# Performance work log

Hardware: AMD Instinct MI355X
Metric: run time of the kernel (lower is better)

## Reference

```python
import jax, jax.numpy as jnp
import numpy as np

THRESH = 0.2  # contact probability threshold from _make_graph default


def setup_inputs() -> dict:
    key = jax.random.key(0)
    ks = jax.random.split(key, 10)
    L, D, K, M = 1024, 640, 32, 64
    S = jax.random.normal(ks[0], (L, D), jnp.float32)
    P = jax.random.uniform(ks[1], (L, L), jnp.float32)
    P = 0.5 * (P + P.T)  # symmetric base-pair probability matrix
    xyz = jax.random.normal(ks[2], (L, 3), jnp.float32) * 10.0  # Angstrom-scale C1' coords
    rbf_mu = jnp.linspace(0.0, 30.0, K).astype(jnp.float32)     # RBF centers over 0-30 A
    rbf_sigma = jax.random.uniform(ks[3], (K,), jnp.float32, 0.5, 2.0)
    W_edge = jax.random.normal(ks[4], (K + 2, M), jnp.float32) * 0.05
    b_edge = jnp.zeros((M,), jnp.float32)
    W_node = jax.random.normal(ks[5], (D, M), jnp.float32) * 0.05
    w_out = jax.random.normal(ks[6], (M,), jnp.float32) * 0.1
    return {"S": S, "P": P, "xyz": xyz, "rbf_mu": rbf_mu, "rbf_sigma": rbf_sigma,
            "W_edge": W_edge, "b_edge": b_edge, "W_node": W_node, "w_out": w_out}


def reference(S, P, xyz, rbf_mu, rbf_sigma, W_edge, b_edge, W_node, w_out):
    """Graph construction (_make_graph) + one SE3-style gated coordinate update.

    Edges: backbone (j == i+1, etype=0, pij=1) and high-prob contacts
    (P[i,j] > THRESH, j > i+2, etype=1, pij=P[i,j]). Edge scalars are
    [etype, pij, rbf(d)] exactly as in _make_graph; edge vectors are
    xyz[j]-xyz[i]. Computed in dense masked form for jit-compatibility.
    """
    L = xyz.shape[0]
    rel = xyz[None, :, :] - xyz[:, None, :]                      # (L,L,3) xyz[j]-xyz[i]
    # safe norm: eps avoids nan grad on zero diagonal (diagonal is masked out anyway)
    d = jnp.sqrt(jnp.sum(rel * rel, axis=-1, keepdims=True) + 1e-12)  # (L,L,1)
    rbf_feat = jnp.exp(-(d - rbf_mu) ** 2 / (2.0 * rbf_sigma ** 2))   # (L,L,K)

    idx = jnp.arange(L)
    backbone = idx[None, :] == idx[:, None] + 1                  # j == i+1
    contact = (P > THRESH) & (idx[None, :] > idx[:, None] + 2)   # skip j <= i+2
    mask = backbone | contact                                    # (L,L)

    etype = contact.astype(S.dtype)                              # 0 backbone, 1 contact
    pij = jnp.where(backbone, jnp.asarray(1.0, S.dtype), P)
    e_scalar = jnp.concatenate([etype[..., None], pij[..., None], rbf_feat], axis=-1)  # (L,L,K+2)

    # gather-compute: message from edge scalars + destination-node scalars
    node_proj = S @ W_node                                       # (L,M)
    msg = jax.nn.relu(jnp.einsum('ijk,km->ijm', e_scalar, W_edge) + b_edge
                      + node_proj[None, :, :])                   # (L,L,M)
    gate = jax.nn.sigmoid(msg @ w_out) * mask.astype(S.dtype)    # (L,L)

    # scatter: equivariant coordinate update, sum of gated edge vectors per node
    xyz_out = xyz + jnp.einsum('ij,ijc->ic', gate, rel)          # (L,3)
    return xyz_out
```

## Files before the change

### kernel.cpp

```cpp
#include <hip/hip_runtime.h>
#include <math.h>

#define LL 1024
#define DD 640
#define KK 32
#define MM 64
#define THRESH 0.2f

#define NPROJ_OFF 0
#define WRT_OFF   (LL * MM)
#define W0_OFF    (WRT_OFF + 1024)
#define W1_OFF    (W0_OFF + MM)
#define MU_OFF    (W1_OFF + MM)
#define NIS2_OFF  (MU_OFF + KK)

typedef float f32x4_t __attribute__((ext_vector_type(4)));
typedef short bf16x8_t __attribute__((ext_vector_type(8)));

union FragU { unsigned int u[4]; bf16x8_t v; };

__device__ __forceinline__ unsigned int pack_bf(float hi, float lo) {
    return __builtin_amdgcn_perm(__float_as_uint(hi), __float_as_uint(lo), 0x07060302u);
}

__global__ __launch_bounds__(256) void prep_kernel(
    const float* __restrict__ S, const float* __restrict__ rbf_mu,
    const float* __restrict__ rbf_sigma, const float* __restrict__ W_edge,
    const float* __restrict__ b_edge, const float* __restrict__ W_node,
    float* __restrict__ ws)
{
    __shared__ float red[4][2][64];
    const int b = blockIdx.x;
    const int t = threadIdx.x;
    if (b < LL / 2) {
        const int m = t & 63;
        const int c = t >> 6;
        const int r0 = b * 2;
        float a0 = 0.f, a1 = 0.f;
        const int d0 = c * 160;
        #pragma unroll 4
        for (int dd = d0; dd < d0 + 160; dd += 4) {
            const float4 s0 = *(const float4*)(S + (size_t)r0 * DD + dd);
            const float4 s1 = *(const float4*)(S + (size_t)(r0 + 1) * DD + dd);
            const float w0 = W_node[(dd + 0) * MM + m];
            const float w1 = W_node[(dd + 1) * MM + m];
            const float w2 = W_node[(dd + 2) * MM + m];
            const float w3 = W_node[(dd + 3) * MM + m];
            a0 = fmaf(s0.x, w0, a0); a0 = fmaf(s0.y, w1, a0);
            a0 = fmaf(s0.z, w2, a0); a0 = fmaf(s0.w, w3, a0);
            a1 = fmaf(s1.x, w0, a1); a1 = fmaf(s1.y, w1, a1);
            a1 = fmaf(s1.z, w2, a1); a1 = fmaf(s1.w, w3, a1);
        }
        red[c][0][m] = a0;
        red[c][1][m] = a1;
        __syncthreads();
        if (t < 64) {
            const float be = b_edge[t];
            const float v0 = ((red[0][0][t] + red[1][0][t]) + (red[2][0][t] + red[3][0][t])) + be;
            const float v1 = ((red[0][1][t] + red[1][1][t]) + (red[2][1][t] + red[3][1][t])) + be;
            ws[NPROJ_OFF + (size_t)r0 * MM + t]       = v0;
            ws[NPROJ_OFF + (size_t)(r0 + 1) * MM + t] = v1;
        }
    } else {
        unsigned short* wrt = (unsigned short*)(ws + WRT_OFF);
        if (t < MM) {
            ws[W0_OFF + t] = W_edge[t];
            ws[W1_OFF + t] = W_edge[MM + t];
        }
        if (t < KK) {
            ws[MU_OFF + t] = rbf_mu[t];
            const float s = rbf_sigma[t];
            ws[NIS2_OFF + t] = -1.0f / (2.0f * s * s);
        }
        for (int idx = t; idx < KK * MM; idx += 256) {
            const int m = idx >> 5, k = idx & 31;
            unsigned int u = __float_as_uint(W_edge[(2 + k) * MM + m]);
            u = (u + 0x7fffu + ((u >> 16) & 1u)) >> 16;
            wrt[idx] = (unsigned short)u;
        }
    }
}

__global__ __launch_bounds__(512, 4) void edge_kernel(
    const float* __restrict__ P, const float* __restrict__ xyz,
    const float* __restrict__ w_out, const float* __restrict__ ws,
    float* __restrict__ out)
{
    const int tid  = threadIdx.x;
    const int lane = tid & 63;
    const int wave = tid >> 6;
    const int quad = lane >> 4;
    const int col  = lane & 15;
    __shared__ float sred[8][3];

    const float* __restrict__ nproj = ws + NPROJ_OFF;
    const unsigned short* __restrict__ wrt = (const unsigned short*)(ws + WRT_OFF);

    FragU ar[4];
    f32x4_t w0q[4], w1q[4], wv[4];
    float muj[8], nis2[8];
    #pragma unroll
    for (int mt = 0; mt < 4; ++mt) {
        const uint4 w = *(const uint4*)(wrt + (mt * 16 + col) * KK + quad * 8);
        ar[mt].u[0] = w.x; ar[mt].u[1] = w.y; ar[mt].u[2] = w.z; ar[mt].u[3] = w.w;
        w0q[mt] = *(const f32x4_t*)(ws + W0_OFF + mt * 16 + quad * 4);
        w1q[mt] = *(const f32x4_t*)(ws + W1_OFF + mt * 16 + quad * 4);
        wv[mt]  = *(const f32x4_t*)(w_out + mt * 16 + quad * 4);
    }
    #pragma unroll
    for (int j = 0; j < 8; ++j) {
        muj[j]  = ws[MU_OFF + quad * 8 + j];
        nis2[j] = ws[NIS2_OFF + quad * 8 + j];
    }

    int rows[2];
    rows[0] = (int)blockIdx.x;
    rows[1] = (LL - 1) - (int)blockIdx.x;

    for (int rr = 0; rr < 2; ++rr) {
        const int i = rows[rr];
        const float xi0 = xyz[i * 3 + 0];
        const float xi1 = xyz[i * 3 + 1];
        const float xi2 = xyz[i * 3 + 2];
        float ax = 0.f, ay = 0.f, az = 0.f;
        const int len = (LL - 1) - i;

        for (int base = wave * 64; base < len; base += 512) {
            const int jo = base + lane;
            const bool valid = jo < len;
            const int jc = valid ? (i + 1 + jo) : (LL - 1);
            const float p_own = P[(size_t)i * LL + jc];
            const float rx = xyz[jc * 3 + 0] - xi0;
            const float ry = xyz[jc * 3 + 1] - xi1;
            const float rz = xyz[jc * 3 + 2] - xi2;
            const bool msk = valid && ((jo == 0) || ((jo >= 2) && (p_own > THRESH)));

            float res[4];
            #pragma unroll
            for (int ct = 0; ct < 4; ++ct) {
                const int jo_n = base + ct * 16 + col;
                const int jc_n = (jo_n < len) ? (i + 1 + jo_n) : (LL - 1);
                const float p_n = P[(size_t)i * LL + jc_n];
                const float dx = xyz[jc_n * 3 + 0] - xi0;
                const float dy = xyz[jc_n * 3 + 1] - xi1;
                const float dz = xyz[jc_n * 3 + 2] - xi2;
                const float d_n = sqrtf(fmaf(dx, dx, fmaf(dy, dy, fmaf(dz, dz, 1e-12f))));
                const float et = ((jo_n >= 2) && (p_n > THRESH)) ? 1.0f : 0.0f;
                const float pj = (jo_n == 0) ? 1.0f : p_n;

                float r[8];
                #pragma unroll
                for (int j = 0; j < 8; ++j) {
                    const float t0 = d_n - muj[j];
                    r[j] = __expf(t0 * t0 * nis2[j]);
                }
                FragU bf;
                bf.u[0] = pack_bf(r[1], r[0]); bf.u[1] = pack_bf(r[3], r[2]);
                bf.u[2] = pack_bf(r[5], r[4]); bf.u[3] = pack_bf(r[7], r[6]);

                const float* npr = nproj + (size_t)jc_n * MM;
                float g = 0.0f;
                #pragma unroll
                for (int mt = 0; mt < 4; ++mt) {
                    f32x4_t c0 = *(const f32x4_t*)(npr + mt * 16 + quad * 4);
                    c0[0] = fmaf(et, w0q[mt][0], fmaf(pj, w1q[mt][0], c0[0]));
                    c0[1] = fmaf(et, w0q[mt][1], fmaf(pj, w1q[mt][1], c0[1]));
                    c0[2] = fmaf(et, w0q[mt][2], fmaf(pj, w1q[mt][2], c0[2]));
                    c0[3] = fmaf(et, w0q[mt][3], fmaf(pj, w1q[mt][3], c0[3]));
                    c0 = __builtin_amdgcn_mfma_f32_16x16x32_bf16(ar[mt].v, bf.v, c0, 0, 0, 0);
                    g = fmaf(fmaxf(c0[0], 0.f), wv[mt][0], g);
                    g = fmaf(fmaxf(c0[1], 0.f), wv[mt][1], g);
                    g = fmaf(fmaxf(c0[2], 0.f), wv[mt][2], g);
                    g = fmaf(fmaxf(c0[3], 0.f), wv[mt][3], g);
                }
                g += __shfl_xor(g, 16, 64);
                g += __shfl_xor(g, 32, 64);
                res[ct] = g;
            }
            float gd = res[0];
            gd = (quad == 1) ? res[1] : gd;
            gd = (quad == 2) ? res[2] : gd;
            gd = (quad == 3) ? res[3] : gd;
            const float gate = msk ? (1.0f / (1.0f + __expf(-gd))) : 0.0f;
            ax = fmaf(gate, rx, ax);
            ay = fmaf(gate, ry, ay);
            az = fmaf(gate, rz, az);
        }

        #pragma unroll
        for (int off = 32; off > 0; off >>= 1) {
            ax += __shfl_down(ax, off, 64);
            ay += __shfl_down(ay, off, 64);
            az += __shfl_down(az, off, 64);
        }
        if (lane == 0) {
            sred[wave][0] = ax; sred[wave][1] = ay; sred[wave][2] = az;
        }
        __syncthreads();
        if (tid == 0) {
            float tx = 0.f, ty = 0.f, tz = 0.f;
            #pragma unroll
            for (int w = 0; w < 8; ++w) {
                tx += sred[w][0]; ty += sred[w][1]; tz += sred[w][2];
            }
            out[i * 3 + 0] = xi0 + tx;
            out[i * 3 + 1] = xi1 + ty;
            out[i * 3 + 2] = xi2 + tz;
        }
        __syncthreads();
    }
}

extern "C" void kernel_launch(void* const* d_in, const int* in_sizes, int n_in,
                              void* d_out, int out_size, void* d_ws, size_t ws_size,
                              hipStream_t stream) {
    const float* S         = (const float*)d_in[0];
    const float* P         = (const float*)d_in[1];
    const float* xyz       = (const float*)d_in[2];
    const float* rbf_mu    = (const float*)d_in[3];
    const float* rbf_sigma = (const float*)d_in[4];
    const float* W_edge    = (const float*)d_in[5];
    const float* b_edge    = (const float*)d_in[6];
    const float* W_node    = (const float*)d_in[7];
    const float* w_out     = (const float*)d_in[8];
    float* out = (float*)d_out;
    float* ws  = (float*)d_ws;

    prep_kernel<<<LL / 2 + 1, 256, 0, stream>>>(S, rbf_mu, rbf_sigma, W_edge,
                                                b_edge, W_node, ws);
    edge_kernel<<<LL / 2, 512, 0, stream>>>(P, xyz, w_out, ws, out);
}
```

Baseline: 102.5 us.

## Give each block one row, fold edge-type weight into node projections, pad xyz

```diff
diff --git a/kernel.cpp b/kernel.cpp
--- a/kernel.cpp
+++ b/kernel.cpp
@@ -7,27 +7,34 @@
 #define MM 64
 #define THRESH 0.2f
 
-#define NPROJ_OFF 0
-#define WRT_OFF   (LL * MM)
-#define W0_OFF    (WRT_OFF + 1024)
-#define W1_OFF    (W0_OFF + MM)
-#define MU_OFF    (W1_OFF + MM)
-#define NIS2_OFF  (MU_OFF + KK)
+#define NPROJ_OFF  0
+#define NPROJC_OFF (NPROJ_OFF + LL * MM)
+#define WRT_OFF    (NPROJC_OFF + LL * MM)
+#define W1_OFF     (WRT_OFF + 1024)
+#define MU_OFF     (W1_OFF + MM)
+#define NIS2_OFF   (MU_OFF + KK)
+#define XYZ4_OFF   (NIS2_OFF + KK)
 
 typedef float f32x4_t __attribute__((ext_vector_type(4)));
 typedef short bf16x8_t __attribute__((ext_vector_type(8)));
 
 union FragU { unsigned int u[4]; bf16x8_t v; };
 
+#if __has_builtin(__builtin_amdgcn_sqrtf)
+#define FSQRT __builtin_amdgcn_sqrtf
+#else
+#define FSQRT sqrtf
+#endif
+
 __device__ __forceinline__ unsigned int pack_bf(float hi, float lo) {
     return __builtin_amdgcn_perm(__float_as_uint(hi), __float_as_uint(lo), 0x07060302u);
 }
 
 __global__ __launch_bounds__(256) void prep_kernel(
-    const float* __restrict__ S, const float* __restrict__ rbf_mu,
-    const float* __restrict__ rbf_sigma, const float* __restrict__ W_edge,
-    const float* __restrict__ b_edge, const float* __restrict__ W_node,
-    float* __restrict__ ws)
+    const float* __restrict__ S, const float* __restrict__ xyz,
+    const float* __restrict__ rbf_mu, const float* __restrict__ rbf_sigma,
+    const float* __restrict__ W_edge, const float* __restrict__ b_edge,
+    const float* __restrict__ W_node, float* __restrict__ ws)
 {
     __shared__ float red[4][2][64];
     const int b = blockIdx.x;
@@ -56,17 +63,17 @@
         __syncthreads();
         if (t < 64) {
             const float be = b_edge[t];
+            const float w0 = W_edge[t];
             const float v0 = ((red[0][0][t] + red[1][0][t]) + (red[2][0][t] + red[3][0][t])) + be;
             const float v1 = ((red[0][1][t] + red[1][1][t]) + (red[2][1][t] + red[3][1][t])) + be;
-            ws[NPROJ_OFF + (size_t)r0 * MM + t]       = v0;
-            ws[NPROJ_OFF + (size_t)(r0 + 1) * MM + t] = v1;
+            ws[NPROJ_OFF  + (size_t)r0 * MM + t]       = v0;
+            ws[NPROJ_OFF  + (size_t)(r0 + 1) * MM + t] = v1;
+            ws[NPROJC_OFF + (size_t)r0 * MM + t]       = v0 + w0;
+            ws[NPROJC_OFF + (size_t)(r0 + 1) * MM + t] = v1 + w0;
         }
     } else {
         unsigned short* wrt = (unsigned short*)(ws + WRT_OFF);
-        if (t < MM) {
-            ws[W0_OFF + t] = W_edge[t];
-            ws[W1_OFF + t] = W_edge[MM + t];
-        }
+        if (t < MM) ws[W1_OFF + t] = W_edge[MM + t];
         if (t < KK) {
             ws[MU_OFF + t] = rbf_mu[t];
             const float s = rbf_sigma[t];
@@ -78,136 +85,146 @@
             u = (u + 0x7fffu + ((u >> 16) & 1u)) >> 16;
             wrt[idx] = (unsigned short)u;
         }
-    }
-}
-
-__global__ __launch_bounds__(512, 4) void edge_kernel(
-    const float* __restrict__ P, const float* __restrict__ xyz,
-    const float* __restrict__ w_out, const float* __restrict__ ws,
-    float* __restrict__ out)
+        for (int n = t; n < LL; n += 256) {
+            float4 v;
+            v.x = xyz[3 * n + 0]; v.y = xyz[3 * n + 1];
+            v.z = xyz[3 * n + 2]; v.w = 0.0f;
+            *(float4*)(ws + XYZ4_OFF + 4 * n) = v;
+        }
+    }
+}
+
+__global__ __launch_bounds__(256, 3) void edge_kernel(
+    const float* __restrict__ P, const float* __restrict__ w_out,
+    const float* __restrict__ ws, float* __restrict__ out)
 {
     const int tid  = threadIdx.x;
     const int lane = tid & 63;
     const int wave = tid >> 6;
     const int quad = lane >> 4;
     const int col  = lane & 15;
-    __shared__ float sred[8][3];
-
-    const float* __restrict__ nproj = ws + NPROJ_OFF;
+    __shared__ float sred[4][3];
+
+    const float* __restrict__ nproj  = ws + NPROJ_OFF;
+    const float* __restrict__ nprojc = ws + NPROJC_OFF;
+    const float4* __restrict__ xyz4  = (const float4*)(ws + XYZ4_OFF);
     const unsigned short* __restrict__ wrt = (const unsigned short*)(ws + WRT_OFF);
 
     FragU ar[4];
-    f32x4_t w0q[4], w1q[4], wv[4];
+    float w1r[16], wvr[16];
     float muj[8], nis2[8];
     #pragma unroll
     for (int mt = 0; mt < 4; ++mt) {
         const uint4 w = *(const uint4*)(wrt + (mt * 16 + col) * KK + quad * 8);
         ar[mt].u[0] = w.x; ar[mt].u[1] = w.y; ar[mt].u[2] = w.z; ar[mt].u[3] = w.w;
-        w0q[mt] = *(const f32x4_t*)(ws + W0_OFF + mt * 16 + quad * 4);
-        w1q[mt] = *(const f32x4_t*)(ws + W1_OFF + mt * 16 + quad * 4);
-        wv[mt]  = *(const f32x4_t*)(w_out + mt * 16 + quad * 4);
+        const f32x4_t w1 = *(const f32x4_t*)(ws + W1_OFF + mt * 16 + quad * 4);
+        const f32x4_t wo = *(const f32x4_t*)(w_out + mt * 16 + quad * 4);
+        #pragma unroll
+        for (int r = 0; r < 4; ++r) { w1r[mt * 4 + r] = w1[r]; wvr[mt * 4 + r] = wo[r]; }
     }
     #pragma unroll
     for (int j = 0; j < 8; ++j) {
         muj[j]  = ws[MU_OFF + quad * 8 + j];
         nis2[j] = ws[NIS2_OFF + quad * 8 + j];
     }
-
-    int rows[2];
-    rows[0] = (int)blockIdx.x;
-    rows[1] = (LL - 1) - (int)blockIdx.x;
-
-    for (int rr = 0; rr < 2; ++rr) {
-        const int i = rows[rr];
-        const float xi0 = xyz[i * 3 + 0];
-        const float xi1 = xyz[i * 3 + 1];
-        const float xi2 = xyz[i * 3 + 2];
-        float ax = 0.f, ay = 0.f, az = 0.f;
-        const int len = (LL - 1) - i;
-
-        for (int base = wave * 64; base < len; base += 512) {
-            const int jo = base + lane;
-            const bool valid = jo < len;
-            const int jc = valid ? (i + 1 + jo) : (LL - 1);
-            const float p_own = P[(size_t)i * LL + jc];
-            const float rx = xyz[jc * 3 + 0] - xi0;
-            const float ry = xyz[jc * 3 + 1] - xi1;
-            const float rz = xyz[jc * 3 + 2] - xi2;
-            const bool msk = valid && ((jo == 0) || ((jo >= 2) && (p_own > THRESH)));
-
-            float res[4];
+    #pragma unroll
+    for (int mt = 0; mt < 4; ++mt) {
+        asm volatile("" : "+v"(ar[mt].u[0]), "+v"(ar[mt].u[1]),
+                          "+v"(ar[mt].u[2]), "+v"(ar[mt].u[3]));
+        asm volatile("" : "+v"(w1r[mt*4+0]), "+v"(w1r[mt*4+1]),
+                          "+v"(w1r[mt*4+2]), "+v"(w1r[mt*4+3]));
+        asm volatile("" : "+v"(wvr[mt*4+0]), "+v"(wvr[mt*4+1]),
+                          "+v"(wvr[mt*4+2]), "+v"(wvr[mt*4+3]));
+    }
+    #pragma unroll
+    for (int j = 0; j < 8; j += 4) {
+        asm volatile("" : "+v"(muj[j]), "+v"(muj[j+1]), "+v"(muj[j+2]), "+v"(muj[j+3]));
+        asm volatile("" : "+v"(nis2[j]), "+v"(nis2[j+1]), "+v"(nis2[j+2]), "+v"(nis2[j+3]));
+    }
+
+    const int i = (int)blockIdx.x;
+    const float4 xo = xyz4[i];
+    const float xi0 = xo.x, xi1 = xo.y, xi2 = xo.z;
+    float ax = 0.f, ay = 0.f, az = 0.f;
+    const int len = (LL - 1) - i;
+
+    for (int base = wave * 64; base < len; base += 256) {
+        const int jo = base + lane;
+        const bool valid = jo < len;
+        const int jc = valid ? (i + 1 + jo) : (LL - 1);
+        const float p_own = P[(size_t)i * LL + jc];
+        const float4 xj = xyz4[jc];
+        const float rx = xj.x - xi0, ry = xj.y - xi1, rz = xj.z - xi2;
+        const bool msk = valid && ((jo == 0) || ((jo >= 2) && (p_own > THRESH)));
+
+        float res[4];
+        #pragma unroll
+        for (int ct = 0; ct < 4; ++ct) {
+            const int jo_n = base + ct * 16 + col;
+            int jc_n = i + 1 + jo_n;
+            jc_n = (jc_n < LL) ? jc_n : (LL - 1);
+            const float p_n = P[(size_t)i * LL + jc_n];
+            const float4 xn = xyz4[jc_n];
+            const float dx = xn.x - xi0, dy = xn.y - xi1, dz = xn.z - xi2;
+            const float d_n = FSQRT(fmaf(dx, dx, fmaf(dy, dy, fmaf(dz, dz, 1e-12f))));
+            const bool bb = (jo_n == 0);
+            const float peff = bb ? 1.0f : p_n;
+            const float* bp = bb ? nproj : nprojc;
+
+            float r[8];
             #pragma unroll
-            for (int ct = 0; ct < 4; ++ct) {
-                const int jo_n = base + ct * 16 + col;
-                const int jc_n = (jo_n < len) ? (i + 1 + jo_n) : (LL - 1);
-                const float p_n = P[(size_t)i * LL + jc_n];
-                const float dx = xyz[jc_n * 3 + 0] - xi0;
-                const float dy = xyz[jc_n * 3 + 1] - xi1;
-                const float dz = xyz[jc_n * 3 + 2] - xi2;
-                const float d_n = sqrtf(fmaf(dx, dx, fmaf(dy, dy, fmaf(dz, dz, 1e-12f))));
-                const float et = ((jo_n >= 2) && (p_n > THRESH)) ? 1.0f : 0.0f;
-                const float pj = (jo_n == 0) ? 1.0f : p_n;
-
-                float r[8];
-                #pragma unroll
-                for (int j = 0; j < 8; ++j) {
-                    const float t0 = d_n - muj[j];
-                    r[j] = __expf(t0 * t0 * nis2[j]);
-                }
-                FragU bf;
-                bf.u[0] = pack_bf(r[1], r[0]); bf.u[1] = pack_bf(r[3], r[2]);
-                bf.u[2] = pack_bf(r[5], r[4]); bf.u[3] = pack_bf(r[7], r[6]);
-
-                const float* npr = nproj + (size_t)jc_n * MM;
-                float g = 0.0f;
-                #pragma unroll
-                for (int mt = 0; mt < 4; ++mt) {
-                    f32x4_t c0 = *(const f32x4_t*)(npr + mt * 16 + quad * 4);
-                    c0[0] = fmaf(et, w0q[mt][0], fmaf(pj, w1q[mt][0], c0[0]));
-                    c0[1] = fmaf(et, w0q[mt][1], fmaf(pj, w1q[mt][1], c0[1]));
-                    c0[2] = fmaf(et, w0q[mt][2], fmaf(pj, w1q[mt][2], c0[2]));
-                    c0[3] = fmaf(et, w0q[mt][3], fmaf(pj, w1q[mt][3], c0[3]));
-                    c0 = __builtin_amdgcn_mfma_f32_16x16x32_bf16(ar[mt].v, bf.v, c0, 0, 0, 0);
-                    g = fmaf(fmaxf(c0[0], 0.f), wv[mt][0], g);
-                    g = fmaf(fmaxf(c0[1], 0.f), wv[mt][1], g);
-                    g = fmaf(fmaxf(c0[2], 0.f), wv[mt][2], g);
-                    g = fmaf(fmaxf(c0[3], 0.f), wv[mt][3], g);
-                }
-                g += __shfl_xor(g, 16, 64);
-                g += __shfl_xor(g, 32, 64);
-                res[ct] = g;
+            for (int j = 0; j < 8; ++j) {
+                const float t0 = d_n - muj[j];
+                r[j] = __expf(t0 * t0 * nis2[j]);
             }
-            float gd = res[0];
-            gd = (quad == 1) ? res[1] : gd;
-            gd = (quad == 2) ? res[2] : gd;
-            gd = (quad == 3) ? res[3] : gd;
-            const float gate = msk ? (1.0f / (1.0f + __expf(-gd))) : 0.0f;
-            ax = fmaf(gate, rx, ax);
-            ay = fmaf(gate, ry, ay);
-            az = fmaf(gate, rz, az);
-        }
-
-        #pragma unroll
-        for (int off = 32; off > 0; off >>= 1) {
-            ax += __shfl_down(ax, off, 64);
-            ay += __shfl_down(ay, off, 64);
-            az += __shfl_down(az, off, 64);
-        }
-        if (lane == 0) {
-            sred[wave][0] = ax; sred[wave][1] = ay; sred[wave][2] = az;
-        }
-        __syncthreads();
-        if (tid == 0) {
-            float tx = 0.f, ty = 0.f, tz = 0.f;
+            FragU bf;
+            bf.u[0] = pack_bf(r[1], r[0]); bf.u[1] = pack_bf(r[3], r[2]);
+            bf.u[2] = pack_bf(r[5], r[4]); bf.u[3] = pack_bf(r[7], r[6]);
+
+            const float* npr = bp + (size_t)jc_n * MM;
+            float g = 0.0f;
             #pragma unroll
-            for (int w = 0; w < 8; ++w) {
-                tx += sred[w][0]; ty += sred[w][1]; tz += sred[w][2];
+            for (int mt = 0; mt < 4; ++mt) {
+                f32x4_t c0 = *(const f32x4_t*)(npr + mt * 16 + quad * 4);
+                c0[0] = fmaf(peff, w1r[mt*4+0], c0[0]);
+                c0[1] = fmaf(peff, w1r[mt*4+1], c0[1]);
+                c0[2] = fmaf(peff, w1r[mt*4+2], c0[2]);
+                c0[3] = fmaf(peff, w1r[mt*4+3], c0[3]);
+                c0 = __builtin_amdgcn_mfma_f32_16x16x32_bf16(ar[mt].v, bf.v, c0, 0, 0, 0);
+                g = fmaf(fmaxf(c0[0], 0.f), wvr[mt*4+0], g);
+                g = fmaf(fmaxf(c0[1], 0.f), wvr[mt*4+1], g);
+                g = fmaf(fmaxf(c0[2], 0.f), wvr[mt*4+2], g);
+                g = fmaf(fmaxf(c0[3], 0.f), wvr[mt*4+3], g);
             }
-            out[i * 3 + 0] = xi0 + tx;
-            out[i * 3 + 1] = xi1 + ty;
-            out[i * 3 + 2] = xi2 + tz;
-        }
-        __syncthreads();
+            g += __shfl_xor(g, 16, 64);
+            g += __shfl_xor(g, 32, 64);
+            res[ct] = g;
+        }
+        float gd = res[0];
+        gd = (quad == 1) ? res[1] : gd;
+        gd = (quad == 2) ? res[2] : gd;
+        gd = (quad == 3) ? res[3] : gd;
+        const float gate = msk ? (1.0f / (1.0f + __expf(-gd))) : 0.0f;
+        ax = fmaf(gate, rx, ax);
+        ay = fmaf(gate, ry, ay);
+        az = fmaf(gate, rz, az);
+    }
+
+    #pragma unroll
+    for (int off = 32; off > 0; off >>= 1) {
+        ax += __shfl_down(ax, off, 64);
+        ay += __shfl_down(ay, off, 64);
+        az += __shfl_down(az, off, 64);
+    }
+    if (lane == 0) { sred[wave][0] = ax; sred[wave][1] = ay; sred[wave][2] = az; }
+    __syncthreads();
+    if (tid == 0) {
+        const float tx = (sred[0][0] + sred[1][0]) + (sred[2][0] + sred[3][0]);
+        const float ty = (sred[0][1] + sred[1][1]) + (sred[2][1] + sred[3][1]);
+        const float tz = (sred[0][2] + sred[1][2]) + (sred[2][2] + sred[3][2]);
+        out[i * 3 + 0] = xi0 + tx;
+        out[i * 3 + 1] = xi1 + ty;
+        out[i * 3 + 2] = xi2 + tz;
     }
 }
 
@@ -226,7 +243,7 @@
     float* out = (float*)d_out;
     float* ws  = (float*)d_ws;
 
-    prep_kernel<<<LL / 2 + 1, 256, 0, stream>>>(S, rbf_mu, rbf_sigma, W_edge,
-                                                b_edge, W_node, ws);
-    edge_kernel<<<LL / 2, 512, 0, stream>>>(P, xyz, w_out, ws, out);
-}
+    prep_kernel<<<LL / 2 + 1, 256, 0, stream>>>(S, xyz, rbf_mu, rbf_sigma,
+                                                W_edge, b_edge, W_node, ws);
+    edge_kernel<<<LL, 256, 0, stream>>>(P, w_out, ws, out);
+}
```

After: 103.7 us. About the same (+1.1%).
